# Optimization experiments

Measured on AMD Instinct MI355X. Metric: run time of the kernel, lower is better.

Reference implementation:

```python
import jax, jax.numpy as jnp
import numpy as np

N, E, IN_DIM, HID = 100000, 1600000, 128, 64


def setup_inputs() -> dict:
    key = jax.random.key(0)
    ks = jax.random.split(key, 10)
    inv = lambda f: 1.0 / np.sqrt(f)
    return {
        "x": jax.random.normal(ks[0], (N, IN_DIM), jnp.float32),
        "edge_index": jax.random.randint(ks[1], (2, E), 0, N, dtype=jnp.int32),
        "fc_w": jax.random.normal(ks[2], (IN_DIM, HID), jnp.float32) * inv(IN_DIM),
        "fc_b": jnp.zeros((HID,), jnp.float32),
        "conv1_w": jax.random.normal(ks[3], (HID, HID), jnp.float32) * inv(HID),
        "conv1_b": jnp.zeros((HID,), jnp.float32),
        "conv2_w": jax.random.normal(ks[4], (HID, HID), jnp.float32) * inv(HID),
        "conv2_b": jnp.zeros((HID,), jnp.float32),
        "node_w": jax.random.normal(ks[5], (HID, 1), jnp.float32) * inv(HID),
        "node_b": jnp.zeros((1,), jnp.float32),
        "edge_w": jax.random.normal(ks[6], (2 * HID, 1), jnp.float32) * inv(2 * HID),
        "edge_b": jnp.zeros((1,), jnp.float32),
    }


def _gcn_norm(row, col):
    # PyG GCNConv default: add self-loops, symmetric D^-1/2 (A+I) D^-1/2 norm.
    loops = jnp.arange(N, dtype=row.dtype)
    rows = jnp.concatenate([row, loops])
    cols = jnp.concatenate([col, loops])
    deg = jax.ops.segment_sum(jnp.ones(rows.shape[0], jnp.float32), cols, num_segments=N)
    dinv = jax.lax.rsqrt(jnp.maximum(deg, 1.0))  # deg >= 1 due to self-loops
    norm = dinv[rows] * dinv[cols]  # [E+N]
    return rows, cols, norm


def _gcn_conv(h, rows, cols, norm, W, b):
    m = h @ W                                   # [N, HID] transform first (out==in dim)
    agg = jax.ops.segment_sum(m[rows] * norm[:, None], cols, num_segments=N)
    return agg + b


def reference(x, edge_index, fc_w, fc_b, conv1_w, conv1_b, conv2_w, conv2_b,
              node_w, node_b, edge_w, edge_b):
    # Dropout layers act as identity in eval mode.
    row, col = edge_index[0], edge_index[1]
    rows, cols, norm = _gcn_norm(row, col)

    h = x @ fc_w + fc_b                          # [N, HID]
    h = jax.nn.relu(_gcn_conv(h, rows, cols, norm, conv1_w, conv1_b))
    h = jax.nn.relu(_gcn_conv(h, rows, cols, norm, conv2_w, conv2_b))

    node_score = jax.nn.sigmoid(h @ node_w + node_b)  # [N, 1]

    # edge_score = sigmoid(cat([h[row], h[col]]) @ edge_w + b)
    # == sigmoid(h[row] @ edge_w[:HID] + h[col] @ edge_w[HID:] + b)
    s_src = h @ edge_w[:HID]                     # [N, 1]
    s_dst = h @ edge_w[HID:]                     # [N, 1]
    edge_score = jax.nn.sigmoid(s_src[row] + s_dst[col] + edge_b)  # [E, 1]
    return edge_score, node_score
```

## Files before the change

### kernel.cpp

```cpp
#include <hip/hip_runtime.h>
#include <math.h>

constexpr int NN  = 100000;
constexpr int EE  = 1600000;
constexpr int IND = 128;
constexpr int HID = 64;

constexpr int NBUCK = (NN + 127) / 128;
constexpr int CAP   = 2432;
constexpr int CHUNK = 4096;
constexpr int NTILE = NN / 16;

using bf16x8 = __attribute__((ext_vector_type(8))) short;
using f32x4v = __attribute__((ext_vector_type(4))) float;

__device__ __forceinline__ unsigned short f2bf(float f) {
    union { float f; unsigned int u; } v; v.f = f;
    unsigned int r = (v.u + 0x7FFFu + ((v.u >> 16) & 1u)) >> 16;
    return (unsigned short)r;
}
__device__ __forceinline__ void unp(unsigned int u, float& lo, float& hi) {
    union { unsigned int x; float f; } a, c;
    a.x = u << 16; c.x = u & 0xFFFF0000u;
    lo = a.f; hi = c.f;
}

#define ACC4(u) do { float l_, h_; \
    unp((u).x, l_, h_); a0 += l_; a1 += h_; \
    unp((u).y, l_, h_); a2 += l_; a3 += h_; } while (0)


__global__ __launch_bounds__(256) void k_zero(int* __restrict__ p, int n) {
    int i = blockIdx.x * 256 + threadIdx.x;
    if (i < n) p[i] = 0;
}


__global__ __launch_bounds__(256) void k_bscatter(const int* __restrict__ row, const int* __restrict__ col,
                                                  int* __restrict__ gcur, int* __restrict__ ebuf) {
    __shared__ int lhist[NBUCK];
    __shared__ int lbase[NBUCK];
    __shared__ int lcur[NBUCK];
    const int tx = threadIdx.x;
    const int cbase = blockIdx.x * CHUNK;

    for (int b = tx; b < NBUCK; b += 256) lhist[b] = 0;
    __syncthreads();

    #pragma unroll
    for (int i = 0; i < CHUNK / 256; ++i) {
        int e = cbase + tx + i * 256;
        if (e < EE) atomicAdd(&lhist[col[e] >> 7], 1);
    }
    __syncthreads();

    for (int b = tx; b < NBUCK; b += 256) {
        int c = lhist[b];
        if (c) lbase[b] = atomicAdd(&gcur[b], c);
        lcur[b] = 0;
    }
    __syncthreads();

    #pragma unroll
    for (int i = 0; i < CHUNK / 256; ++i) {
        int e = cbase + tx + i * 256;
        if (e < EE) {
            int c = col[e];
            int b = c >> 7;
            int rank = atomicAdd(&lcur[b], 1);
            ebuf[b * CAP + lbase[b] + rank] = (row[e] << 7) | (c & 127);
        }
    }
}


__global__ __launch_bounds__(256) void k_bsortip(const int* __restrict__ gcur, int* __restrict__ ebuf,
                                                 int* __restrict__ bc, float* __restrict__ dinv) {
    __shared__ int ebl[CAP];
    __shared__ int h[128];
    __shared__ int sc[128];
    __shared__ int cur[128];
    const int tx = threadIdx.x;
    const int b = blockIdx.x;
    const int cnt = gcur[b];
    int* eb = ebuf + b * CAP;

    if (tx < 128) h[tx] = 0;
    for (int e = tx; e < cnt; e += 256) ebl[e] = eb[e];
    __syncthreads();
    for (int e = tx; e < cnt; e += 256) atomicAdd(&h[ebl[e] & 127], 1);
    __syncthreads();

    if (tx < 128) sc[tx] = h[tx];
    __syncthreads();
    #pragma unroll
    for (int o = 1; o < 128; o <<= 1) {
        int add = (tx < 128 && tx >= o) ? sc[tx - o] : 0;
        __syncthreads();
        if (tx < 128) sc[tx] += add;
        __syncthreads();
    }
    if (tx < 128) {
        int ex = sc[tx] - h[tx];
        cur[tx] = ex;
        int g = b * 128 + tx;
        if (g < NN) {
            bc[g]   = (ex << 16) | h[tx];
            dinv[g] = rsqrtf((float)(h[tx] + 1));
        }
    }
    __syncthreads();

    for (int e = tx; e < cnt; e += 256) {
        int v = ebl[e];
        int r = atomicAdd(&cur[v & 127], 1);
        eb[r] = v >> 7;
    }
}


__global__ __launch_bounds__(256) void k_wc(const float* __restrict__ wfc, const float* __restrict__ bfc,
                                            const float* __restrict__ w1,
                                            unsigned short* __restrict__ wct, float* __restrict__ bvec) {
    int b = blockIdx.x, tx = threadIdx.x;
    if (b < 32) {
        int idx = b * 256 + tx;
        int k = idx >> 6, c = idx & 63;
        float acc = 0.f;
        #pragma unroll 8
        for (int j = 0; j < 64; ++j) acc += wfc[k * HID + j] * w1[j * HID + c];
        wct[c * IND + k] = f2bf(acc);
    } else if (tx < 64) {
        float acc = 0.f;
        #pragma unroll 8
        for (int j = 0; j < 64; ++j) acc += bfc[j] * w1[j * HID + tx];
        bvec[tx] = acc;
    }
}


__global__ __launch_bounds__(256) void k_mmx(const float* __restrict__ x,
        const unsigned short* __restrict__ wct, const float* __restrict__ bvec,
        const float* __restrict__ dinv, unsigned short* __restrict__ mdb) {
    const int tx = threadIdx.x;
    const int lane = tx & 63;
    const int wv = tx >> 6;
    const int l15 = lane & 15, g = lane >> 4;
    const int tile = blockIdx.x * 4 + wv;
    if (tile >= NTILE) return;
    const int row0 = tile * 16;

    bf16x8 bf[4][4];
    #pragma unroll
    for (int t = 0; t < 4; ++t) {
        const unsigned short* bp = wct + (t * 16 + l15) * IND + g * 8;
        #pragma unroll
        for (int kc = 0; kc < 4; ++kc)
            bf[t][kc] = *(const bf16x8*)(bp + kc * 32);
    }

    const float* ap = x + (row0 + l15) * IND + g * 8;
    bf16x8 af[4];
    #pragma unroll
    for (int kc = 0; kc < 4; ++kc) {
        float4 lo = *(const float4*)(ap + kc * 32);
        float4 hi = *(const float4*)(ap + kc * 32 + 4);
        bf16x8 f;
        f[0] = (short)f2bf(lo.x); f[1] = (short)f2bf(lo.y);
        f[2] = (short)f2bf(lo.z); f[3] = (short)f2bf(lo.w);
        f[4] = (short)f2bf(hi.x); f[5] = (short)f2bf(hi.y);
        f[6] = (short)f2bf(hi.z); f[7] = (short)f2bf(hi.w);
        af[kc] = f;
    }

    f32x4v acc[4];
    #pragma unroll
    for (int t = 0; t < 4; ++t) {
        float bv = bvec[t * 16 + l15];
        acc[t][0] = bv; acc[t][1] = bv; acc[t][2] = bv; acc[t][3] = bv;
    }
    #pragma unroll
    for (int kc = 0; kc < 4; ++kc) {
        #pragma unroll
        for (int t = 0; t < 4; ++t)
            acc[t] = __builtin_amdgcn_mfma_f32_16x16x32_bf16(af[kc], bf[t][kc], acc[t], 0, 0, 0);
    }

    #pragma unroll
    for (int r = 0; r < 4; ++r) {
        int rowg = row0 + g * 4 + r;
        float di = dinv[rowg];
        #pragma unroll
        for (int t = 0; t < 4; ++t)
            mdb[rowg * HID + t * 16 + l15] = f2bf(acc[t][r] * di);
    }
}


__global__ __launch_bounds__(256) void k_mm(const float* __restrict__ hin, const float* __restrict__ w,
                                            const float* __restrict__ dinv,
                                            unsigned short* __restrict__ mdb) {
    __shared__ float sw[HID * HID];
    const int tx = threadIdx.x;
    for (int i = tx; i < HID * HID; i += 256) sw[i] = w[i];

    const int tc = tx & 15;
    const int gr = tx >> 4;
    const int c0 = tc * 4;
    const int rbase = blockIdx.x * 64 + gr * 4;

    int o[4];
    #pragma unroll
    for (int i = 0; i < 4; ++i) {
        int rg = rbase + i;
        o[i] = (rg < NN ? rg : 0) * HID;
    }
    __syncthreads();

    float acc[4][4] = {};

    #pragma unroll 2
    for (int kk = 0; kk < HID; kk += 4) {
        float4 a[4];
        #pragma unroll
        for (int i = 0; i < 4; ++i) a[i] = *(const float4*)(hin + o[i] + kk);
        float4 b0 = *(const float4*)&sw[(kk + 0) * HID + c0];
        float4 b1 = *(const float4*)&sw[(kk + 1) * HID + c0];
        float4 b2 = *(const float4*)&sw[(kk + 2) * HID + c0];
        float4 b3 = *(const float4*)&sw[(kk + 3) * HID + c0];
        #pragma unroll
        for (int i = 0; i < 4; ++i) {
            acc[i][0] += a[i].x * b0.x + a[i].y * b1.x + a[i].z * b2.x + a[i].w * b3.x;
            acc[i][1] += a[i].x * b0.y + a[i].y * b1.y + a[i].z * b2.y + a[i].w * b3.y;
            acc[i][2] += a[i].x * b0.z + a[i].y * b1.z + a[i].z * b2.z + a[i].w * b3.z;
            acc[i][3] += a[i].x * b0.w + a[i].y * b1.w + a[i].z * b2.w + a[i].w * b3.w;
        }
    }

    #pragma unroll
    for (int i = 0; i < 4; ++i) {
        int rg = rbase + i;
        if (rg < NN) {
            float di = dinv[rg];
            ushort4 o4;
            o4.x = f2bf(acc[i][0] * di); o4.y = f2bf(acc[i][1] * di);
            o4.z = f2bf(acc[i][2] * di); o4.w = f2bf(acc[i][3] * di);
            *(ushort4*)&mdb[rg * HID + c0] = o4;
        }
    }
}


__global__ __launch_bounds__(256) void k_gather(const unsigned short* __restrict__ mdb,
                                                const int* __restrict__ prow, const int* __restrict__ bc,
                                                const float* __restrict__ dinv, const float* __restrict__ b,
                                                float* __restrict__ hout) {
    const uint2* mdq = (const uint2*)mdb;
    int lane = threadIdx.x & 63;
    int q    = lane >> 4;
    int f4   = lane & 15;
    int wid  = (blockIdx.x * blockDim.x + threadIdx.x) >> 6;
    int nwv  = (gridDim.x * blockDim.x) >> 6;
    float4 bj = *(const float4*)&b[f4 * 4];

    for (int i = wid; i < NN; i += nwv) {
        int vv = bc[i];
        int s = (i >> 7) * CAP + (vv >> 16);
        int n = vv & 0xFFFF;
        float a0 = 0.f, a1 = 0.f, a2 = 0.f, a3 = 0.f;
        if (q == 0) {
            uint2 u = mdq[i * 16 + f4];
            ACC4(u);
        }
        for (int e = 0; e < n; e += 16) {
            int e0 = e + q, e1 = e + 4 + q, e2 = e + 8 + q, e3 = e + 12 + q;
            int r0 = prow[s + (e0 < n ? e0 : 0)];
            int r1 = prow[s + (e1 < n ? e1 : 0)];
            int r2 = prow[s + (e2 < n ? e2 : 0)];
            int r3 = prow[s + (e3 < n ? e3 : 0)];
            uint2 u0 = mdq[r0 * 16 + f4];
            uint2 u1 = mdq[r1 * 16 + f4];
            uint2 u2 = mdq[r2 * 16 + f4];
            uint2 u3 = mdq[r3 * 16 + f4];
            if (e1 >= n) { u1.x = 0u; u1.y = 0u; }
            if (e2 >= n) { u2.x = 0u; u2.y = 0u; }
            if (e3 >= n) { u3.x = 0u; u3.y = 0u; }
            if (e0 >= n) { u0.x = 0u; u0.y = 0u; }
            ACC4(u0); ACC4(u1); ACC4(u2); ACC4(u3);
        }
        a0 += __shfl_xor(a0, 32, 64); a1 += __shfl_xor(a1, 32, 64);
        a2 += __shfl_xor(a2, 32, 64); a3 += __shfl_xor(a3, 32, 64);
        a0 += __shfl_xor(a0, 16, 64); a1 += __shfl_xor(a1, 16, 64);
        a2 += __shfl_xor(a2, 16, 64); a3 += __shfl_xor(a3, 16, 64);

        float di = dinv[i];
        float4 o;
        o.x = fmaxf(di * a0 + bj.x, 0.f);
        o.y = fmaxf(di * a1 + bj.y, 0.f);
        o.z = fmaxf(di * a2 + bj.z, 0.f);
        o.w = fmaxf(di * a3 + bj.w, 0.f);
        if (q == 0) *(float4*)&hout[i * HID + f4 * 4] = o;
    }
}


__global__ __launch_bounds__(256) void k_gather2s(const unsigned short* __restrict__ mdb,
        const int* __restrict__ prow, const int* __restrict__ bc, const float* __restrict__ dinv,
        const float* __restrict__ b, const float* __restrict__ nw, const float* __restrict__ nb,
        const float* __restrict__ ew, float* __restrict__ out_node,
        float* __restrict__ ssrc, float* __restrict__ sdst) {
    const uint2* mdq = (const uint2*)mdb;
    int lane = threadIdx.x & 63;
    int q    = lane >> 4;
    int f4   = lane & 15;
    int wid  = (blockIdx.x * blockDim.x + threadIdx.x) >> 6;
    int nwv  = (gridDim.x * blockDim.x) >> 6;
    float4 bj  = *(const float4*)&b[f4 * 4];
    float4 wn  = *(const float4*)&nw[f4 * 4];
    float4 we1 = *(const float4*)&ew[f4 * 4];
    float4 we2 = *(const float4*)&ew[64 + f4 * 4];
    float nb0 = nb[0];

    for (int i = wid; i < NN; i += nwv) {
        int vv = bc[i];
        int s = (i >> 7) * CAP + (vv >> 16);
        int n = vv & 0xFFFF;
        float a0 = 0.f, a1 = 0.f, a2 = 0.f, a3 = 0.f;
        if (q == 0) {
            uint2 u = mdq[i * 16 + f4];
            ACC4(u);
        }
        for (int e = 0; e < n; e += 16) {
            int e0 = e + q, e1 = e + 4 + q, e2 = e + 8 + q, e3 = e + 12 + q;
            int r0 = prow[s + (e0 < n ? e0 : 0)];
            int r1 = prow[s + (e1 < n ? e1 : 0)];
            int r2 = prow[s + (e2 < n ? e2 : 0)];
            int r3 = prow[s + (e3 < n ? e3 : 0)];
            uint2 u0 = mdq[r0 * 16 + f4];
            uint2 u1 = mdq[r1 * 16 + f4];
            uint2 u2 = mdq[r2 * 16 + f4];
            uint2 u3 = mdq[r3 * 16 + f4];
            if (e1 >= n) { u1.x = 0u; u1.y = 0u; }
            if (e2 >= n) { u2.x = 0u; u2.y = 0u; }
            if (e3 >= n) { u3.x = 0u; u3.y = 0u; }
            if (e0 >= n) { u0.x = 0u; u0.y = 0u; }
            ACC4(u0); ACC4(u1); ACC4(u2); ACC4(u3);
        }
        a0 += __shfl_xor(a0, 32, 64); a1 += __shfl_xor(a1, 32, 64);
        a2 += __shfl_xor(a2, 32, 64); a3 += __shfl_xor(a3, 32, 64);
        a0 += __shfl_xor(a0, 16, 64); a1 += __shfl_xor(a1, 16, 64);
        a2 += __shfl_xor(a2, 16, 64); a3 += __shfl_xor(a3, 16, 64);

        float di = dinv[i];
        float v0 = fmaxf(di * a0 + bj.x, 0.f);
        float v1 = fmaxf(di * a1 + bj.y, 0.f);
        float v2 = fmaxf(di * a2 + bj.z, 0.f);
        float v3 = fmaxf(di * a3 + bj.w, 0.f);

        float a  = v0 * wn.x  + v1 * wn.y  + v2 * wn.z  + v3 * wn.w;
        float s1 = v0 * we1.x + v1 * we1.y + v2 * we1.z + v3 * we1.w;
        float s2 = v0 * we2.x + v1 * we2.y + v2 * we2.z + v3 * we2.w;
        #pragma unroll
        for (int off = 8; off; off >>= 1) {
            a  += __shfl_xor(a,  off, 64);
            s1 += __shfl_xor(s1, off, 64);
            s2 += __shfl_xor(s2, off, 64);
        }
        if (lane == 0) {
            out_node[i] = 1.f / (1.f + expf(-(a + nb0)));
            ssrc[i] = s1;
            sdst[i] = s2;
        }
    }
}


__global__ __launch_bounds__(256) void k_edge(const int4* __restrict__ row4, const int4* __restrict__ col4,
                                              const float* __restrict__ ssrc, const float* __restrict__ sdst,
                                              const float* __restrict__ eb, float4* __restrict__ out4) {
    constexpr int NQ = EE / 4;
    int i = blockIdx.x * 256 + threadIdx.x;
    if (i >= NQ) return;
    float eb0 = eb[0];
    int4 r = row4[i], c = col4[i];
    float4 o;
    float z;
    z = ssrc[r.x] + sdst[c.x] + eb0; o.x = 1.f / (1.f + expf(-z));
    z = ssrc[r.y] + sdst[c.y] + eb0; o.y = 1.f / (1.f + expf(-z));
    z = ssrc[r.z] + sdst[c.z] + eb0; o.z = 1.f / (1.f + expf(-z));
    z = ssrc[r.w] + sdst[c.w] + eb0; o.w = 1.f / (1.f + expf(-z));
    out4[i] = o;
}

extern "C" void kernel_launch(void* const* d_in, const int* in_sizes, int n_in,
                              void* d_out, int out_size, void* d_ws, size_t ws_size,
                              hipStream_t stream) {
    const float* x    = (const float*)d_in[0];
    const int*   ei   = (const int*)d_in[1];
    const float* fc_w = (const float*)d_in[2];
    const float* fc_b = (const float*)d_in[3];
    const float* c1w  = (const float*)d_in[4];
    const float* c1b  = (const float*)d_in[5];
    const float* c2w  = (const float*)d_in[6];
    const float* c2b  = (const float*)d_in[7];
    const float* nw   = (const float*)d_in[8];
    const float* nb   = (const float*)d_in[9];
    const float* ew   = (const float*)d_in[10];
    const float* eb   = (const float*)d_in[11];
    const int* row = ei;
    const int* col = ei + EE;

    constexpr int NP = 100352;
    float* ws   = (float*)d_ws;
    float* dinv = ws;
    int*   bc   = (int*)(ws + NP);
    int*   gcur = (int*)(ws + 2 * NP);
    unsigned short* wct = (unsigned short*)(ws + 2 * NP + 1024);
    float* bvec = ws + 2 * NP + 1024 + 4096;
    int*   ebuf = (int*)(bvec + 128);
    float* A    = (float*)(ebuf + NBUCK * CAP);
    unsigned short* Bbf = (unsigned short*)(A + (size_t)NN * HID);
    float* ssrc = A;
    float* sdst = A + NP;

    float* out_edge = (float*)d_out;
    float* out_node = out_edge + EE;

    const int nbG = (NN + 63) / 64;
    const int nbC = (EE + CHUNK - 1) / CHUNK;
    const int nbQ = (EE / 4 + 255) / 256;
    const int nbM = (NTILE + 3) / 4;

    k_zero    <<<(NBUCK + 255) / 256, 256, 0, stream>>>(gcur, NBUCK);
    k_bscatter<<<nbC, 256, 0, stream>>>(row, col, gcur, ebuf);
    k_bsortip <<<NBUCK, 256, 0, stream>>>(gcur, ebuf, bc, dinv);

    k_wc    <<<33, 256, 0, stream>>>(fc_w, fc_b, c1w, wct, bvec);
    k_mmx   <<<nbM, 256, 0, stream>>>(x, wct, bvec, dinv, Bbf);
    k_gather<<<2048, 256, 0, stream>>>(Bbf, ebuf, bc, dinv, c1b, A);

    k_mm      <<<nbG, 256, 0, stream>>>(A, c2w, dinv, Bbf);
    k_gather2s<<<2048, 256, 0, stream>>>(Bbf, ebuf, bc, dinv, c2b,
                                         nw, nb, ew, out_node, ssrc, sdst);

    k_edge<<<nbQ, 256, 0, stream>>>((const int4*)row, (const int4*)col,
                                    ssrc, sdst, eb, (float4*)out_edge);
}
```

Baseline: 195.9 us.

## Store layer-1 output as bf16 and run second transform with MFMA

The first gather now writes its hidden output in bf16 instead of fp32. The second dense transform is replaced by an MFMA bf16 kernel that reads those bf16 rows against a bf16 transposed copy of conv2_w, which is prepared in extra blocks of the weight-combine kernel. This halves the intermediate activation traffic and moves the 64x64 matmul from scalar FMAs onto matrix cores. The cost is an extra bf16 rounding of the hidden activations and conv2 weights.

```diff
diff --git a/kernel.cpp b/kernel.cpp
--- a/kernel.cpp
+++ b/kernel.cpp
@@ -120,8 +120,9 @@
 
 
 __global__ __launch_bounds__(256) void k_wc(const float* __restrict__ wfc, const float* __restrict__ bfc,
-                                            const float* __restrict__ w1,
-                                            unsigned short* __restrict__ wct, float* __restrict__ bvec) {
+                                            const float* __restrict__ w1, const float* __restrict__ w2,
+                                            unsigned short* __restrict__ wct, float* __restrict__ bvec,
+                                            unsigned short* __restrict__ w2t) {
     int b = blockIdx.x, tx = threadIdx.x;
     if (b < 32) {
         int idx = b * 256 + tx;
@@ -130,6 +131,10 @@
         #pragma unroll 8
         for (int j = 0; j < 64; ++j) acc += wfc[k * HID + j] * w1[j * HID + c];
         wct[c * IND + k] = f2bf(acc);
+    } else if (b < 48) {
+        int idx = (b - 32) * 256 + tx;
+        int k = idx >> 6, c = idx & 63;
+        w2t[c * HID + k] = f2bf(w2[k * HID + c]);
     } else if (tx < 64) {
         float acc = 0.f;
         #pragma unroll 8
@@ -197,56 +202,46 @@
 }
 
 
-__global__ __launch_bounds__(256) void k_mm(const float* __restrict__ hin, const float* __restrict__ w,
-                                            const float* __restrict__ dinv,
-                                            unsigned short* __restrict__ mdb) {
-    __shared__ float sw[HID * HID];
+__global__ __launch_bounds__(256) void k_mm2x(const unsigned short* __restrict__ h1b,
+        const unsigned short* __restrict__ w2t, const float* __restrict__ dinv,
+        unsigned short* __restrict__ mdb) {
     const int tx = threadIdx.x;
-    for (int i = tx; i < HID * HID; i += 256) sw[i] = w[i];
-
-    const int tc = tx & 15;
-    const int gr = tx >> 4;
-    const int c0 = tc * 4;
-    const int rbase = blockIdx.x * 64 + gr * 4;
-
-    int o[4];
-    #pragma unroll
-    for (int i = 0; i < 4; ++i) {
-        int rg = rbase + i;
-        o[i] = (rg < NN ? rg : 0) * HID;
-    }
-    __syncthreads();
-
-    float acc[4][4] = {};
-
-    #pragma unroll 2
-    for (int kk = 0; kk < HID; kk += 4) {
-        float4 a[4];
-        #pragma unroll
-        for (int i = 0; i < 4; ++i) a[i] = *(const float4*)(hin + o[i] + kk);
-        float4 b0 = *(const float4*)&sw[(kk + 0) * HID + c0];
-        float4 b1 = *(const float4*)&sw[(kk + 1) * HID + c0];
-        float4 b2 = *(const float4*)&sw[(kk + 2) * HID + c0];
-        float4 b3 = *(const float4*)&sw[(kk + 3) * HID + c0];
-        #pragma unroll
-        for (int i = 0; i < 4; ++i) {
-            acc[i][0] += a[i].x * b0.x + a[i].y * b1.x + a[i].z * b2.x + a[i].w * b3.x;
-            acc[i][1] += a[i].x * b0.y + a[i].y * b1.y + a[i].z * b2.y + a[i].w * b3.y;
-            acc[i][2] += a[i].x * b0.z + a[i].y * b1.z + a[i].z * b2.z + a[i].w * b3.z;
-            acc[i][3] += a[i].x * b0.w + a[i].y * b1.w + a[i].z * b2.w + a[i].w * b3.w;
-        }
-    }
-
-    #pragma unroll
-    for (int i = 0; i < 4; ++i) {
-        int rg = rbase + i;
-        if (rg < NN) {
-            float di = dinv[rg];
-            ushort4 o4;
-            o4.x = f2bf(acc[i][0] * di); o4.y = f2bf(acc[i][1] * di);
-            o4.z = f2bf(acc[i][2] * di); o4.w = f2bf(acc[i][3] * di);
-            *(ushort4*)&mdb[rg * HID + c0] = o4;
-        }
+    const int lane = tx & 63;
+    const int wv = tx >> 6;
+    const int l15 = lane & 15, g = lane >> 4;
+    const int tile = blockIdx.x * 4 + wv;
+    if (tile >= NTILE) return;
+    const int row0 = tile * 16;
+
+    bf16x8 bf[4][2];
+    #pragma unroll
+    for (int t = 0; t < 4; ++t) {
+        const unsigned short* bp = w2t + (t * 16 + l15) * HID + g * 8;
+        #pragma unroll
+        for (int kc = 0; kc < 2; ++kc)
+            bf[t][kc] = *(const bf16x8*)(bp + kc * 32);
+    }
+
+    const unsigned short* ap = h1b + (row0 + l15) * HID + g * 8;
+    bf16x8 af[2];
+    af[0] = *(const bf16x8*)(ap);
+    af[1] = *(const bf16x8*)(ap + 32);
+
+    f32x4v acc[4] = {};
+    #pragma unroll
+    for (int kc = 0; kc < 2; ++kc) {
+        #pragma unroll
+        for (int t = 0; t < 4; ++t)
+            acc[t] = __builtin_amdgcn_mfma_f32_16x16x32_bf16(af[kc], bf[t][kc], acc[t], 0, 0, 0);
+    }
+
+    #pragma unroll
+    for (int r = 0; r < 4; ++r) {
+        int rowg = row0 + g * 4 + r;
+        float di = dinv[rowg];
+        #pragma unroll
+        for (int t = 0; t < 4; ++t)
+            mdb[rowg * HID + t * 16 + l15] = f2bf(acc[t][r] * di);
     }
 }
 
@@ -254,7 +249,7 @@
 __global__ __launch_bounds__(256) void k_gather(const unsigned short* __restrict__ mdb,
                                                 const int* __restrict__ prow, const int* __restrict__ bc,
                                                 const float* __restrict__ dinv, const float* __restrict__ b,
-                                                float* __restrict__ hout) {
+                                                unsigned short* __restrict__ hout) {
     const uint2* mdq = (const uint2*)mdb;
     int lane = threadIdx.x & 63;
     int q    = lane >> 4;
@@ -294,12 +289,14 @@
         a2 += __shfl_xor(a2, 16, 64); a3 += __shfl_xor(a3, 16, 64);
 
         float di = dinv[i];
-        float4 o;
-        o.x = fmaxf(di * a0 + bj.x, 0.f);
-        o.y = fmaxf(di * a1 + bj.y, 0.f);
-        o.z = fmaxf(di * a2 + bj.z, 0.f);
-        o.w = fmaxf(di * a3 + bj.w, 0.f);
-        if (q == 0) *(float4*)&hout[i * HID + f4 * 4] = o;
+        if (q == 0) {
+            ushort4 o;
+            o.x = f2bf(fmaxf(di * a0 + bj.x, 0.f));
+            o.y = f2bf(fmaxf(di * a1 + bj.y, 0.f));
+            o.z = f2bf(fmaxf(di * a2 + bj.z, 0.f));
+            o.w = f2bf(fmaxf(di * a3 + bj.w, 0.f));
+            *(ushort4*)&hout[i * HID + f4 * 4] = o;
+        }
     }
 }
 
@@ -417,16 +414,17 @@
     int*   gcur = (int*)(ws + 2 * NP);
     unsigned short* wct = (unsigned short*)(ws + 2 * NP + 1024);
     float* bvec = ws + 2 * NP + 1024 + 4096;
-    int*   ebuf = (int*)(bvec + 128);
-    float* A    = (float*)(ebuf + NBUCK * CAP);
-    unsigned short* Bbf = (unsigned short*)(A + (size_t)NN * HID);
-    float* ssrc = A;
-    float* sdst = A + NP;
+    unsigned short* w2t = (unsigned short*)(bvec + 128);
+    int*   ebuf = (int*)(bvec + 128 + 2048);
+    float* Areg = (float*)(ebuf + NBUCK * CAP);
+    unsigned short* h1b = (unsigned short*)Areg;
+    unsigned short* Bbf = (unsigned short*)(Areg + (size_t)NN * HID / 2);
+    float* ssrc = Areg;
+    float* sdst = Areg + NP;
 
     float* out_edge = (float*)d_out;
     float* out_node = out_edge + EE;
 
-    const int nbG = (NN + 63) / 64;
     const int nbC = (EE + CHUNK - 1) / CHUNK;
     const int nbQ = (EE / 4 + 255) / 256;
     const int nbM = (NTILE + 3) / 4;
@@ -435,11 +433,11 @@
     k_bscatter<<<nbC, 256, 0, stream>>>(row, col, gcur, ebuf);
     k_bsortip <<<NBUCK, 256, 0, stream>>>(gcur, ebuf, bc, dinv);
 
-    k_wc    <<<33, 256, 0, stream>>>(fc_w, fc_b, c1w, wct, bvec);
+    k_wc    <<<49, 256, 0, stream>>>(fc_w, fc_b, c1w, c2w, wct, bvec, w2t);
     k_mmx   <<<nbM, 256, 0, stream>>>(x, wct, bvec, dinv, Bbf);
-    k_gather<<<2048, 256, 0, stream>>>(Bbf, ebuf, bc, dinv, c1b, A);
-
-    k_mm      <<<nbG, 256, 0, stream>>>(A, c2w, dinv, Bbf);
+    k_gather<<<2048, 256, 0, stream>>>(Bbf, ebuf, bc, dinv, c1b, h1b);
+
+    k_mm2x    <<<nbM, 256, 0, stream>>>(h1b, w2t, dinv, Bbf);
     k_gather2s<<<2048, 256, 0, stream>>>(Bbf, ebuf, bc, dinv, c2b,
                                          nw, nb, ew, out_node, ssrc, sdst);
 
```

After: 187.2 us. 1.05x faster.
